# Performance work log

Hardware: AMD Instinct MI355X
Metric: run time of the kernel (lower is better)

The kernel has to match this reference:

```python
import jax, jax.numpy as jnp
import numpy as np

EMB = 1024
HEADS = 16
DFF = 4096
EPS = 1e-6


def _linear_params(key, din, dout):
    kw, kb = jax.random.split(key)
    w = jax.random.normal(kw, (din, dout), jnp.float32) * (1.0 / np.sqrt(din))
    b = jax.random.normal(kb, (dout,), jnp.float32) * 0.01
    return w, b


def setup_inputs() -> dict:
    key = jax.random.key(0)
    ks = jax.random.split(key, 8)
    x = jax.random.normal(ks[0], (2, 2048, EMB), jnp.float32)
    Wq, bq = _linear_params(ks[1], EMB, EMB)
    Wk, bk = _linear_params(ks[2], EMB, EMB)
    Wv, bv = _linear_params(ks[3], EMB, EMB)
    W1, b1 = _linear_params(ks[4], EMB, DFF)
    W2, b2 = _linear_params(ks[5], DFF, EMB)
    g1 = jnp.ones((EMB,), jnp.float32)
    be1 = jnp.zeros((EMB,), jnp.float32)
    g2 = jnp.ones((EMB,), jnp.float32)
    be2 = jnp.zeros((EMB,), jnp.float32)
    return dict(x=x, Wq=Wq, bq=bq, Wk=Wk, bk=bk, Wv=Wv, bv=bv,
                g1=g1, be1=be1, g2=g2, be2=be2, W1=W1, b1=b1, W2=W2, b2=b2)


def _layernorm(x, g, b):
    mu = jnp.mean(x, axis=-1, keepdims=True)
    var = jnp.mean(jnp.square(x - mu), axis=-1, keepdims=True)
    return (x - mu) * jax.lax.rsqrt(var + EPS) * g + b


def reference(x, Wq, bq, Wk, bk, Wv, bv, g1, be1, g2, be2, W1, b1, W2, b2):
    b, n, d = x.shape
    dh = d // HEADS
    res = x
    h = _layernorm(x, g1, be1)
    # q/k/v projections, split heads: [b, n, H, dh]
    q = (h @ Wq + bq).reshape(b, n, HEADS, dh)
    k = (h @ Wk + bk).reshape(b, n, HEADS, dh)
    v = (h @ Wv + bv).reshape(b, n, HEADS, dh)
    # NOTE: original code applies NO 1/sqrt(dh) scaling
    scores = jnp.einsum('bnhd,bmhd->bhnm', q, k)
    attn = jax.nn.softmax(scores, axis=-1)
    out = jnp.einsum('bhnm,bmhd->bnhd', attn, v).reshape(b, n, d)
    out = out + res  # no output projection in original module
    res = out
    h = _layernorm(out, g2, be2)
    h = jax.nn.gelu(h @ W1 + b1, approximate=False)
    h = h @ W2 + b2
    return h + res
```

## Files before the change

kernel.cpp:

```cpp
#include <hip/hip_runtime.h>
#include <math.h>

#define EMB 1024
#define HEADS 16
#define DH 64
#define DFF 4096
#define NTOK 2048
#define BATCH 2
#define MROWS 4096

typedef __attribute__((ext_vector_type(8))) _Float16 f16x8;
typedef __attribute__((ext_vector_type(4))) float floatx4;

typedef const __attribute__((address_space(1))) void gas_void;
typedef __attribute__((address_space(3))) void las_void;

__device__ __forceinline__ unsigned short f2h(float f) {
    union { _Float16 h; unsigned short u; } c; c.h = (_Float16)f; return c.u;
}
__device__ __forceinline__ float h2f(unsigned short u) {
    union { _Float16 h; unsigned short u; } c; c.u = u; return (float)c.h;
}

__global__ __launch_bounds__(256) void bias_prep(
    const float* __restrict__ bq, const float* __restrict__ bk,
    const float* __restrict__ bv, const float* __restrict__ b1,
    const float* __restrict__ b2, float* __restrict__ out)
{
    int i = blockIdx.x * 256 + threadIdx.x;
    float v;
    if (i < 1024)      v = bq[i];
    else if (i < 2048) v = bk[i - 1024];
    else if (i < 3072) v = bv[i - 2048];
    else if (i < 7168) v = b1[i - 3072];
    else               v = b2[i - 7168];
    out[i] = v;
}

__global__ __launch_bounds__(256) void transpose_f2h(
    const float* __restrict__ in, int ld_in,
    unsigned short* __restrict__ out, int ld_out)
{
    __shared__ unsigned short tile[64][72];
    const int t = threadIdx.x;
    const int r0 = blockIdx.y * 64, c0 = blockIdx.x * 64;
    const int rr = t >> 4, c4 = (t & 15) * 4;
#pragma unroll
    for (int p = 0; p < 4; p++) {
        float4 v = *(const float4*)&in[(size_t)(r0 + rr + p * 16) * ld_in + c0 + c4];
        tile[rr + p * 16][c4 + 0] = f2h(v.x);
        tile[rr + p * 16][c4 + 1] = f2h(v.y);
        tile[rr + p * 16][c4 + 2] = f2h(v.z);
        tile[rr + p * 16][c4 + 3] = f2h(v.w);
    }
    __syncthreads();
#pragma unroll
    for (int p = 0; p < 4; p++) {
        const int c = rr + p * 16;
        ushort4 v;
        v.x = tile[c4 + 0][c]; v.y = tile[c4 + 1][c];
        v.z = tile[c4 + 2][c]; v.w = tile[c4 + 3][c];
        *(ushort4*)&out[(size_t)(c0 + c) * ld_out + r0 + c4] = v;
    }
}

__global__ __launch_bounds__(256) void vtrans(
    const unsigned short* __restrict__ qkv, unsigned short* __restrict__ vT)
{
    __shared__ unsigned short tile[64][72];
    const int t = threadIdx.x;
    const int n0 = blockIdx.x * 64;
    const int bh = blockIdx.y;
    const int b = bh >> 4, h = bh & 15;
    const int rr = t >> 4, c4 = (t & 15) * 4;
    const unsigned short* src = qkv + (size_t)b * NTOK * 3072 + 2048 + h * 64;
#pragma unroll
    for (int p = 0; p < 4; p++) {
        ushort4 v = *(const ushort4*)&src[(size_t)(n0 + rr + p * 16) * 3072 + c4];
        *(ushort4*)&tile[rr + p * 16][c4] = v;
    }
    __syncthreads();
    unsigned short* dst = vT + (size_t)bh * 64 * NTOK;
#pragma unroll
    for (int p = 0; p < 4; p++) {
        const int d = rr + p * 16;
        ushort4 v;
        v.x = tile[c4 + 0][d]; v.y = tile[c4 + 1][d];
        v.z = tile[c4 + 2][d]; v.w = tile[c4 + 3][d];
        *(ushort4*)&dst[(size_t)d * NTOK + n0 + c4] = v;
    }
}

__global__ __launch_bounds__(256) void ln_kernel(
    const float* __restrict__ in,
    const float* __restrict__ g,
    const float* __restrict__ be,
    unsigned short* __restrict__ out)
{
    const int row = blockIdx.x, t = threadIdx.x;
    const size_t base = (size_t)row * 1024 + t * 4;
    float4 xv = *(const float4*)&in[base];
    float v0 = xv.x, v1 = xv.y, v2 = xv.z, v3 = xv.w;
    float s = v0 + v1 + v2 + v3;
    float q = v0 * v0 + v1 * v1 + v2 * v2 + v3 * v3;
#pragma unroll
    for (int m = 1; m < 64; m <<= 1) { s += __shfl_xor(s, m, 64); q += __shfl_xor(q, m, 64); }
    __shared__ float red[8];
    if ((t & 63) == 0) { red[t >> 6] = s; red[4 + (t >> 6)] = q; }
    __syncthreads();
    s = red[0] + red[1] + red[2] + red[3];
    q = red[4] + red[5] + red[6] + red[7];
    const float mu = s * (1.f / 1024.f);
    const float var = q * (1.f / 1024.f) - mu * mu;
    const float rs = rsqrtf(var + 1e-6f);
    float4 gv = *(const float4*)&g[t * 4];
    float4 bv = *(const float4*)&be[t * 4];
    ushort4 ov;
    ov.x = f2h((v0 - mu) * rs * gv.x + bv.x);
    ov.y = f2h((v1 - mu) * rs * gv.y + bv.y);
    ov.z = f2h((v2 - mu) * rs * gv.z + bv.z);
    ov.w = f2h((v3 - mu) * rs * gv.w + bv.w);
    *(ushort4*)&out[base] = ov;
}

template<int EPI, typename CT>
__global__ __launch_bounds__(256) void gemm_f16(
    const unsigned short* __restrict__ A, int lda,
    const unsigned short* __restrict__ Bt, int ldb,
    const float* __restrict__ bias,
    const float* __restrict__ resid,
    CT* __restrict__ C, int ldc, int K)
{
    __shared__ unsigned short As[128 * 64];
    __shared__ unsigned short Bs[128 * 64];
    const int t = threadIdx.x;
    const int l = t & 63, w = t >> 6;
    const int wr = w >> 1, wc = w & 1;
    const int lr = l & 15, lg = l >> 4;
    const int m0 = blockIdx.y * 128, n0 = blockIdx.x * 128;

    const int srow = t >> 3;
    const int scol = (t & 7) * 8;
    const unsigned short* ga0 = A + (size_t)(m0 + srow) * lda + scol;
    const unsigned short* gb0 = Bt + (size_t)(n0 + srow) * ldb + scol;
    const int ldsbase = w * 512;

    floatx4 acc[4][4];
#pragma unroll
    for (int a = 0; a < 4; a++)
#pragma unroll
        for (int b = 0; b < 4; b++) acc[a][b] = (floatx4){0.f, 0.f, 0.f, 0.f};

    for (int k0 = 0; k0 < K; k0 += 64) {
#pragma unroll
        for (int i = 0; i < 4; i++)
            __builtin_amdgcn_global_load_lds((gas_void*)(ga0 + (size_t)i * 32 * lda + k0),
                                             (las_void*)(As + i * 2048 + ldsbase), 16, 0, 0);
#pragma unroll
        for (int i = 0; i < 4; i++)
            __builtin_amdgcn_global_load_lds((gas_void*)(gb0 + (size_t)i * 32 * ldb + k0),
                                             (las_void*)(Bs + i * 2048 + ldsbase), 16, 0, 0);
        __syncthreads();
#pragma unroll
        for (int kf = 0; kf < 2; kf++) {
            f16x8 af[4], bfr[4];
#pragma unroll
            for (int a = 0; a < 4; a++)
                af[a] = *(const f16x8*)&As[(wr * 64 + a * 16 + lr) * 64 + kf * 32 + lg * 8];
#pragma unroll
            for (int b = 0; b < 4; b++)
                bfr[b] = *(const f16x8*)&Bs[(wc * 64 + b * 16 + lr) * 64 + kf * 32 + lg * 8];
#pragma unroll
            for (int a = 0; a < 4; a++)
#pragma unroll
                for (int b = 0; b < 4; b++)
                    acc[a][b] = __builtin_amdgcn_mfma_f32_16x16x32_f16(af[a], bfr[b], acc[a][b], 0, 0, 0);
        }
        __syncthreads();
    }

#pragma unroll
    for (int a = 0; a < 4; a++) {
        const int row0 = m0 + wr * 64 + a * 16 + lg * 4;
#pragma unroll
        for (int b = 0; b < 4; b++) {
            const int col = n0 + wc * 64 + b * 16 + lr;
            const float bs = bias[col];
#pragma unroll
            for (int r = 0; r < 4; r++) {
                float v = acc[a][b][r] + bs;
                if (EPI == 1) v = 0.5f * v * (1.0f + erff(v * 0.70710678118654752f));
                const size_t idx = (size_t)(row0 + r) * ldc + col;
                if (EPI == 2) v += resid[idx];
                if (sizeof(CT) == 2) C[idx] = (CT)f2h(v);
                else                 C[idx] = (CT)v;
            }
        }
    }
}

__global__ __launch_bounds__(256) void attn_kernel(
    const unsigned short* __restrict__ qkv,
    const unsigned short* __restrict__ vT,
    const float* __restrict__ x,
    float* __restrict__ y)
{
    __shared__ unsigned short P[4][32 * 32];
    const int t = threadIdx.x;
    const int l = t & 63, w = t >> 6;
    const int lr = l & 15, lg = l >> 4;
    const int qb = blockIdx.x, bh = blockIdx.y;
    const int b = bh >> 4, h = bh & 15;
    const int q0 = qb * 128 + w * 32;

    const unsigned short* qbase = qkv + (size_t)b * NTOK * 3072 + h * 64;
    const unsigned short* kbase = qbase + 1024;
    const unsigned short* vbase = vT + (size_t)bh * 64 * NTOK;

    f16x8 qf[2][2];
#pragma unroll
    for (int mf = 0; mf < 2; mf++)
#pragma unroll
        for (int kf = 0; kf < 2; kf++)
            qf[mf][kf] = *(const f16x8*)&qbase[(size_t)(q0 + mf * 16 + lr) * 3072 + kf * 32 + lg * 8];

    floatx4 o[2][4];
    float mrun[2][4], lrun[2][4];
#pragma unroll
    for (int mf = 0; mf < 2; mf++) {
#pragma unroll
        for (int df = 0; df < 4; df++) o[mf][df] = (floatx4){0.f, 0.f, 0.f, 0.f};
#pragma unroll
        for (int r = 0; r < 4; r++) { mrun[mf][r] = -1e30f; lrun[mf][r] = 0.f; }
    }

    for (int kt = 0; kt < NTOK; kt += 32) {
        f16x8 kfr[2][2];
#pragma unroll
        for (int n = 0; n < 2; n++)
#pragma unroll
            for (int kf = 0; kf < 2; kf++)
                kfr[n][kf] = *(const f16x8*)&kbase[(size_t)(kt + n * 16 + lr) * 3072 + kf * 32 + lg * 8];

        floatx4 s[2][2];
#pragma unroll
        for (int mf = 0; mf < 2; mf++)
#pragma unroll
            for (int n = 0; n < 2; n++) {
                s[mf][n] = (floatx4){0.f, 0.f, 0.f, 0.f};
                s[mf][n] = __builtin_amdgcn_mfma_f32_16x16x32_f16(qf[mf][0], kfr[n][0], s[mf][n], 0, 0, 0);
                s[mf][n] = __builtin_amdgcn_mfma_f32_16x16x32_f16(qf[mf][1], kfr[n][1], s[mf][n], 0, 0, 0);
            }

#pragma unroll
        for (int mf = 0; mf < 2; mf++) {
#pragma unroll
            for (int r = 0; r < 4; r++) {
                float a0 = s[mf][0][r], a1 = s[mf][1][r];
                float tm = fmaxf(a0, a1);
#pragma unroll
                for (int msk = 1; msk < 16; msk <<= 1) tm = fmaxf(tm, __shfl_xor(tm, msk, 64));
                const float nm = fmaxf(mrun[mf][r], tm);
                const float corr = __expf(mrun[mf][r] - nm);
                mrun[mf][r] = nm;
                const float p0 = __expf(a0 - nm);
                const float p1 = __expf(a1 - nm);
                float rs = p0 + p1;
#pragma unroll
                for (int msk = 1; msk < 16; msk <<= 1) rs += __shfl_xor(rs, msk, 64);
                lrun[mf][r] = lrun[mf][r] * corr + rs;
#pragma unroll
                for (int df = 0; df < 4; df++) o[mf][df][r] *= corr;
                P[w][(mf * 16 + lg * 4 + r) * 32 + lr]      = f2h(p0);
                P[w][(mf * 16 + lg * 4 + r) * 32 + 16 + lr] = f2h(p1);
            }
        }

        f16x8 pa[2];
#pragma unroll
        for (int mf = 0; mf < 2; mf++)
            pa[mf] = *(const f16x8*)&P[w][(mf * 16 + lr) * 32 + lg * 8];
        f16x8 vf[4];
#pragma unroll
        for (int df = 0; df < 4; df++)
            vf[df] = *(const f16x8*)&vbase[(size_t)(df * 16 + lr) * NTOK + kt + lg * 8];
#pragma unroll
        for (int mf = 0; mf < 2; mf++)
#pragma unroll
            for (int df = 0; df < 4; df++)
                o[mf][df] = __builtin_amdgcn_mfma_f32_16x16x32_f16(pa[mf], vf[df], o[mf][df], 0, 0, 0);
    }

#pragma unroll
    for (int mf = 0; mf < 2; mf++)
#pragma unroll
        for (int r = 0; r < 4; r++) {
            const float inv = 1.0f / lrun[mf][r];
            const int row = q0 + mf * 16 + lg * 4 + r;
#pragma unroll
            for (int df = 0; df < 4; df++) {
                const size_t idx = (size_t)(b * NTOK + row) * 1024 + h * 64 + df * 16 + lr;
                y[idx] = o[mf][df][r] * inv + x[idx];
            }
        }
}

extern "C" void kernel_launch(void* const* d_in, const int* in_sizes, int n_in,
                              void* d_out, int out_size, void* d_ws, size_t ws_size,
                              hipStream_t stream)
{
    const float* x   = (const float*)d_in[0];
    const float* Wq  = (const float*)d_in[1];
    const float* bq  = (const float*)d_in[2];
    const float* Wk  = (const float*)d_in[3];
    const float* bk  = (const float*)d_in[4];
    const float* Wv  = (const float*)d_in[5];
    const float* bv  = (const float*)d_in[6];
    const float* g1  = (const float*)d_in[7];
    const float* be1 = (const float*)d_in[8];
    const float* g2  = (const float*)d_in[9];
    const float* be2 = (const float*)d_in[10];
    const float* W1  = (const float*)d_in[11];
    const float* b1  = (const float*)d_in[12];
    const float* W2  = (const float*)d_in[13];
    const float* b2  = (const float*)d_in[14];

    char* ws = (char*)d_ws;
    unsigned short* WqkvT = (unsigned short*)ws;  ws += (size_t)3072 * 1024 * 2;
    unsigned short* W1T   = (unsigned short*)ws;  ws += (size_t)4096 * 1024 * 2;
    unsigned short* W2T   = (unsigned short*)ws;  ws += (size_t)1024 * 4096 * 2;
    float*          biasf = (float*)ws;           ws += (size_t)8192 * 4;
    unsigned short* h1    = (unsigned short*)ws;  ws += (size_t)MROWS * 1024 * 2;
    unsigned short* qkv   = (unsigned short*)ws;  ws += (size_t)MROWS * 3072 * 2;
    unsigned short* vT    = (unsigned short*)ws;  ws += (size_t)32 * 64 * NTOK * 2;
    float*          y     = (float*)ws;           ws += (size_t)MROWS * 1024 * 4;
    unsigned short* act1  = (unsigned short*)ws;  ws += (size_t)MROWS * 4096 * 2;
    unsigned short* h2    = h1;

    bias_prep<<<32, 256, 0, stream>>>(bq, bk, bv, b1, b2, biasf);
    transpose_f2h<<<dim3(16, 16), 256, 0, stream>>>(Wq, 1024, WqkvT, 1024);
    transpose_f2h<<<dim3(16, 16), 256, 0, stream>>>(Wk, 1024, WqkvT + 1024 * 1024, 1024);
    transpose_f2h<<<dim3(16, 16), 256, 0, stream>>>(Wv, 1024, WqkvT + 2 * 1024 * 1024, 1024);
    transpose_f2h<<<dim3(64, 16), 256, 0, stream>>>(W1, 4096, W1T, 1024);
    transpose_f2h<<<dim3(16, 64), 256, 0, stream>>>(W2, 1024, W2T, 4096);

    ln_kernel<<<MROWS, 256, 0, stream>>>(x, g1, be1, h1);
    gemm_f16<0, unsigned short><<<dim3(24, 32), 256, 0, stream>>>(h1, 1024, WqkvT, 1024, biasf, nullptr, qkv, 3072, 1024);
    vtrans<<<dim3(32, 32), 256, 0, stream>>>(qkv, vT);
    attn_kernel<<<dim3(16, 32), 256, 0, stream>>>(qkv, vT, x, y);
    ln_kernel<<<MROWS, 256, 0, stream>>>(y, g2, be2, h2);
    gemm_f16<1, unsigned short><<<dim3(32, 32), 256, 0, stream>>>(h2, 1024, W1T, 1024, biasf + 3072, nullptr, act1, 4096, 1024);
    gemm_f16<2, float><<<dim3(8, 32), 256, 0, stream>>>(act1, 4096, W2T, 4096, biasf + 7168, y, (float*)d_out, 1024, 4096);
}
```

Measured before the change: 508.6 us.

## Shrink attention query tile per wave and widen key tile to 64

Each wave in the attention kernel now processes 16 query rows with 64-key tiles instead of 32 rows with 32-key tiles. The grid doubles to 1024 blocks and launch_bounds requests 4 blocks per CU. This targets higher occupancy and more parallel work to hide load latency, and halves the number of softmax/shuffle iterations per key. The cost is that K/V reuse per wave halves, doubling K and V traffic from L2/global memory. The P scratch row is padded to 72 halves.

```diff
diff --git a/kernel.cpp b/kernel.cpp
--- a/kernel.cpp
+++ b/kernel.cpp
@@ -199,110 +199,93 @@
     }
 }
 
-__global__ __launch_bounds__(256) void attn_kernel(
+__global__ __launch_bounds__(256, 4) void attn_kernel(
     const unsigned short* __restrict__ qkv,
     const unsigned short* __restrict__ vT,
     const float* __restrict__ x,
     float* __restrict__ y)
 {
-    __shared__ unsigned short P[4][32 * 32];
+    __shared__ unsigned short P[4][16 * 72];
     const int t = threadIdx.x;
     const int l = t & 63, w = t >> 6;
     const int lr = l & 15, lg = l >> 4;
     const int qb = blockIdx.x, bh = blockIdx.y;
     const int b = bh >> 4, h = bh & 15;
-    const int q0 = qb * 128 + w * 32;
+    const int q0 = qb * 64 + w * 16;
 
     const unsigned short* qbase = qkv + (size_t)b * NTOK * 3072 + h * 64;
     const unsigned short* kbase = qbase + 1024;
     const unsigned short* vbase = vT + (size_t)bh * 64 * NTOK;
 
-    f16x8 qf[2][2];
-#pragma unroll
-    for (int mf = 0; mf < 2; mf++)
-#pragma unroll
-        for (int kf = 0; kf < 2; kf++)
-            qf[mf][kf] = *(const f16x8*)&qbase[(size_t)(q0 + mf * 16 + lr) * 3072 + kf * 32 + lg * 8];
-
-    floatx4 o[2][4];
-    float mrun[2][4], lrun[2][4];
-#pragma unroll
-    for (int mf = 0; mf < 2; mf++) {
-#pragma unroll
-        for (int df = 0; df < 4; df++) o[mf][df] = (floatx4){0.f, 0.f, 0.f, 0.f};
-#pragma unroll
-        for (int r = 0; r < 4; r++) { mrun[mf][r] = -1e30f; lrun[mf][r] = 0.f; }
-    }
-
-    for (int kt = 0; kt < NTOK; kt += 32) {
-        f16x8 kfr[2][2];
-#pragma unroll
-        for (int n = 0; n < 2; n++)
-#pragma unroll
-            for (int kf = 0; kf < 2; kf++)
-                kfr[n][kf] = *(const f16x8*)&kbase[(size_t)(kt + n * 16 + lr) * 3072 + kf * 32 + lg * 8];
-
-        floatx4 s[2][2];
-#pragma unroll
-        for (int mf = 0; mf < 2; mf++)
-#pragma unroll
-            for (int n = 0; n < 2; n++) {
-                s[mf][n] = (floatx4){0.f, 0.f, 0.f, 0.f};
-                s[mf][n] = __builtin_amdgcn_mfma_f32_16x16x32_f16(qf[mf][0], kfr[n][0], s[mf][n], 0, 0, 0);
-                s[mf][n] = __builtin_amdgcn_mfma_f32_16x16x32_f16(qf[mf][1], kfr[n][1], s[mf][n], 0, 0, 0);
-            }
-
-#pragma unroll
-        for (int mf = 0; mf < 2; mf++) {
-#pragma unroll
-            for (int r = 0; r < 4; r++) {
-                float a0 = s[mf][0][r], a1 = s[mf][1][r];
-                float tm = fmaxf(a0, a1);
-#pragma unroll
-                for (int msk = 1; msk < 16; msk <<= 1) tm = fmaxf(tm, __shfl_xor(tm, msk, 64));
-                const float nm = fmaxf(mrun[mf][r], tm);
-                const float corr = __expf(mrun[mf][r] - nm);
-                mrun[mf][r] = nm;
-                const float p0 = __expf(a0 - nm);
-                const float p1 = __expf(a1 - nm);
-                float rs = p0 + p1;
-#pragma unroll
-                for (int msk = 1; msk < 16; msk <<= 1) rs += __shfl_xor(rs, msk, 64);
-                lrun[mf][r] = lrun[mf][r] * corr + rs;
-#pragma unroll
-                for (int df = 0; df < 4; df++) o[mf][df][r] *= corr;
-                P[w][(mf * 16 + lg * 4 + r) * 32 + lr]      = f2h(p0);
-                P[w][(mf * 16 + lg * 4 + r) * 32 + 16 + lr] = f2h(p1);
-            }
-        }
-
-        f16x8 pa[2];
-#pragma unroll
-        for (int mf = 0; mf < 2; mf++)
-            pa[mf] = *(const f16x8*)&P[w][(mf * 16 + lr) * 32 + lg * 8];
-        f16x8 vf[4];
-#pragma unroll
-        for (int df = 0; df < 4; df++)
-            vf[df] = *(const f16x8*)&vbase[(size_t)(df * 16 + lr) * NTOK + kt + lg * 8];
-#pragma unroll
-        for (int mf = 0; mf < 2; mf++)
-#pragma unroll
-            for (int df = 0; df < 4; df++)
-                o[mf][df] = __builtin_amdgcn_mfma_f32_16x16x32_f16(pa[mf], vf[df], o[mf][df], 0, 0, 0);
-    }
-
-#pragma unroll
-    for (int mf = 0; mf < 2; mf++)
+    f16x8 qf[2];
+#pragma unroll
+    for (int kf = 0; kf < 2; kf++)
+        qf[kf] = *(const f16x8*)&qbase[(size_t)(q0 + lr) * 3072 + kf * 32 + lg * 8];
+
+    floatx4 o[4];
+    float mrun[4], lrun[4];
+#pragma unroll
+    for (int df = 0; df < 4; df++) o[df] = (floatx4){0.f, 0.f, 0.f, 0.f};
+#pragma unroll
+    for (int r = 0; r < 4; r++) { mrun[r] = -1e30f; lrun[r] = 0.f; }
+
+    for (int kt = 0; kt < NTOK; kt += 64) {
+        floatx4 s[4];
+#pragma unroll
+        for (int n = 0; n < 4; n++) {
+            f16x8 k0 = *(const f16x8*)&kbase[(size_t)(kt + n * 16 + lr) * 3072 + lg * 8];
+            f16x8 k1 = *(const f16x8*)&kbase[(size_t)(kt + n * 16 + lr) * 3072 + 32 + lg * 8];
+            s[n] = (floatx4){0.f, 0.f, 0.f, 0.f};
+            s[n] = __builtin_amdgcn_mfma_f32_16x16x32_f16(qf[0], k0, s[n], 0, 0, 0);
+            s[n] = __builtin_amdgcn_mfma_f32_16x16x32_f16(qf[1], k1, s[n], 0, 0, 0);
+        }
+
 #pragma unroll
         for (int r = 0; r < 4; r++) {
-            const float inv = 1.0f / lrun[mf][r];
-            const int row = q0 + mf * 16 + lg * 4 + r;
-#pragma unroll
-            for (int df = 0; df < 4; df++) {
-                const size_t idx = (size_t)(b * NTOK + row) * 1024 + h * 64 + df * 16 + lr;
-                y[idx] = o[mf][df][r] * inv + x[idx];
-            }
-        }
+            float tm = fmaxf(fmaxf(s[0][r], s[1][r]), fmaxf(s[2][r], s[3][r]));
+#pragma unroll
+            for (int msk = 1; msk < 16; msk <<= 1) tm = fmaxf(tm, __shfl_xor(tm, msk, 64));
+            const float nm = fmaxf(mrun[r], tm);
+            const float corr = __expf(mrun[r] - nm);
+            mrun[r] = nm;
+            float p0 = __expf(s[0][r] - nm);
+            float p1 = __expf(s[1][r] - nm);
+            float p2 = __expf(s[2][r] - nm);
+            float p3 = __expf(s[3][r] - nm);
+            float rs = (p0 + p1) + (p2 + p3);
+#pragma unroll
+            for (int msk = 1; msk < 16; msk <<= 1) rs += __shfl_xor(rs, msk, 64);
+            lrun[r] = lrun[r] * corr + rs;
+#pragma unroll
+            for (int df = 0; df < 4; df++) o[df][r] *= corr;
+            const int prow = (lg * 4 + r) * 72;
+            P[w][prow + lr]      = f2h(p0);
+            P[w][prow + 16 + lr] = f2h(p1);
+            P[w][prow + 32 + lr] = f2h(p2);
+            P[w][prow + 48 + lr] = f2h(p3);
+        }
+
+        f16x8 pa0 = *(const f16x8*)&P[w][lr * 72 + lg * 8];
+        f16x8 pa1 = *(const f16x8*)&P[w][lr * 72 + 32 + lg * 8];
+#pragma unroll
+        for (int df = 0; df < 4; df++) {
+            f16x8 v0 = *(const f16x8*)&vbase[(size_t)(df * 16 + lr) * NTOK + kt + lg * 8];
+            f16x8 v1 = *(const f16x8*)&vbase[(size_t)(df * 16 + lr) * NTOK + kt + 32 + lg * 8];
+            o[df] = __builtin_amdgcn_mfma_f32_16x16x32_f16(pa0, v0, o[df], 0, 0, 0);
+            o[df] = __builtin_amdgcn_mfma_f32_16x16x32_f16(pa1, v1, o[df], 0, 0, 0);
+        }
+    }
+
+#pragma unroll
+    for (int r = 0; r < 4; r++) {
+        const float inv = 1.0f / lrun[r];
+        const int row = q0 + lg * 4 + r;
+#pragma unroll
+        for (int df = 0; df < 4; df++) {
+            const size_t idx = (size_t)(b * NTOK + row) * 1024 + h * 64 + df * 16 + lr;
+            y[idx] = o[df][r] * inv + x[idx];
+        }
+    }
 }
 
 extern "C" void kernel_launch(void* const* d_in, const int* in_sizes, int n_in,
@@ -347,7 +330,7 @@
     ln_kernel<<<MROWS, 256, 0, stream>>>(x, g1, be1, h1);
     gemm_f16<0, unsigned short><<<dim3(24, 32), 256, 0, stream>>>(h1, 1024, WqkvT, 1024, biasf, nullptr, qkv, 3072, 1024);
     vtrans<<<dim3(32, 32), 256, 0, stream>>>(qkv, vT);
-    attn_kernel<<<dim3(16, 32), 256, 0, stream>>>(qkv, vT, x, y);
+    attn_kernel<<<dim3(32, 32), 256, 0, stream>>>(qkv, vT, x, y);
     ln_kernel<<<MROWS, 256, 0, stream>>>(y, g2, be2, h2);
     gemm_f16<1, unsigned short><<<dim3(32, 32), 256, 0, stream>>>(h2, 1024, W1T, 1024, biasf + 3072, nullptr, act1, 4096, 1024);
     gemm_f16<2, float><<<dim3(8, 32), 256, 0, stream>>>(act1, 4096, W2T, 4096, biasf + 7168, y, (float*)d_out, 1024, 4096);
```

New measurement: 590.2 us. 16.1% more time.
